# Kernel tuning notes

Measured on AMD Instinct MI355X. Metric: run time of the kernel, lower is better.

The kernel has to match this reference:

```python
import jax, jax.numpy as jnp
import numpy as np

B = 65536
PEP, TCR, D, FF = 384, 480, 128, 512
H1, H2, OUT = 128, 64, 1
EPS = 1e-5


def _ln(x, g, b):
    mu = jnp.mean(x, axis=-1, keepdims=True)
    var = jnp.mean((x - mu) ** 2, axis=-1, keepdims=True)
    return (x - mu) * jax.lax.rsqrt(var + EPS) * g + b


def _bn(x, g, b):
    # training-mode BatchNorm1d: batch-wide stats, biased variance
    mu = jnp.mean(x, axis=0, keepdims=True)
    var = jnp.mean((x - mu) ** 2, axis=0, keepdims=True)
    return (x - mu) * jax.lax.rsqrt(var + EPS) * g + b


def setup_inputs() -> dict:
    key = jax.random.key(0)
    ks = iter(jax.random.split(key, 40))

    def w(shape, fan):
        s = float(np.sqrt(6.0 / fan))
        return jax.random.uniform(next(ks), shape, jnp.float32, -s, s)

    inp = {
        "x": jax.random.normal(next(ks), (B, PEP + TCR), jnp.float32),
        "w_pep": w((D, PEP), PEP + D), "b_pep": jnp.zeros(D),
        "w_tcr": w((D, TCR), TCR + D), "b_tcr": jnp.zeros(D),
        "wv_p2t": w((D, D), 2 * D), "bv_p2t": jnp.zeros(D),
        "wo_p2t": w((D, D), 2 * D), "bo_p2t": jnp.zeros(D),
        "wv_t2p": w((D, D), 2 * D), "bv_t2p": jnp.zeros(D),
        "wo_t2p": w((D, D), 2 * D), "bo_t2p": jnp.zeros(D),
        "ln_g1p": jnp.ones(D), "ln_b1p": jnp.zeros(D),
        "ln_g2p": jnp.ones(D), "ln_b2p": jnp.zeros(D),
        "ln_g1t": jnp.ones(D), "ln_b1t": jnp.zeros(D),
        "ln_g2t": jnp.ones(D), "ln_b2t": jnp.zeros(D),
        "ffn_w1p": w((FF, D), D + FF), "ffn_b1p": jnp.zeros(FF),
        "ffn_w2p": w((D, FF), D + FF), "ffn_b2p": jnp.zeros(D),
        "ffn_w1t": w((FF, D), D + FF), "ffn_b1t": jnp.zeros(FF),
        "ffn_w2t": w((D, FF), D + FF), "ffn_b2t": jnp.zeros(D),
        "w_h1": w((H1, 2 * D), 2 * D + H1), "b_h1": jnp.zeros(H1),
        "bn1_g": jnp.ones(H1), "bn1_b": jnp.zeros(H1),
        "w_h2": w((H2, H1), H1 + H2), "b_h2": jnp.zeros(H2),
        "bn2_g": jnp.ones(H2), "bn2_b": jnp.zeros(H2),
        "w_out": w((OUT, H2), H2 + OUT), "b_out": jnp.zeros(OUT),
    }
    return inp


def reference(x, w_pep, b_pep, w_tcr, b_tcr,
              wv_p2t, bv_p2t, wo_p2t, bo_p2t,
              wv_t2p, bv_t2p, wo_t2p, bo_t2p,
              ln_g1p, ln_b1p, ln_g2p, ln_b2p,
              ln_g1t, ln_b1t, ln_g2t, ln_b2t,
              ffn_w1p, ffn_b1p, ffn_w2p, ffn_b2p,
              ffn_w1t, ffn_b1t, ffn_w2t, ffn_b2t,
              w_h1, b_h1, bn1_g, bn1_b,
              w_h2, b_h2, bn2_g, bn2_b,
              w_out, b_out):
    pep = x[:, :PEP] @ w_pep.T + b_pep   # (B, 128)
    tcr = x[:, PEP:] @ w_tcr.T + b_tcr   # (B, 128)

    # MHA with seq_len=1: softmax over single key == 1 exactly,
    # so attention output = out_proj(v_proj(key/value input)).
    pa = (tcr @ wv_p2t.T + bv_p2t) @ wo_p2t.T + bo_p2t
    pa = _ln(pep + pa, ln_g1p, ln_b1p)
    h = jax.nn.gelu(pa @ ffn_w1p.T + ffn_b1p, approximate=False)
    pa = _ln(pa + h @ ffn_w2p.T + ffn_b2p, ln_g2p, ln_b2p)

    ta = (pep @ wv_t2p.T + bv_t2p) @ wo_t2p.T + bo_t2p
    ta = _ln(tcr + ta, ln_g1t, ln_b1t)
    h = jax.nn.gelu(ta @ ffn_w1t.T + ffn_b1t, approximate=False)
    ta = _ln(ta + h @ ffn_w2t.T + ffn_b2t, ln_g2t, ln_b2t)

    combined = jnp.concatenate([pa, ta], axis=1)  # (B, 256)
    h1 = jax.nn.gelu(_bn(combined @ w_h1.T + b_h1, bn1_g, bn1_b), approximate=False)
    h2 = jax.nn.gelu(_bn(h1 @ w_h2.T + b_h2, bn2_g, bn2_b), approximate=False)
    return h2 @ w_out.T + b_out  # (B, 1)
```

## Files before the change

kernel.cpp:

```cpp
#include <hip/hip_runtime.h>
#include <hip/hip_bf16.h>
#include <math.h>


typedef __attribute__((ext_vector_type(8))) __bf16 bf16x8;
typedef __attribute__((ext_vector_type(8))) short s16x8;
typedef __attribute__((ext_vector_type(4))) float f32x4;

union S8U { s16x8 s; bf16x8 b; };

__device__ __forceinline__ short f2b(float f) {
  union { float f; unsigned u; } v; v.f = f;
  unsigned r = v.u + 0x7fffu + ((v.u >> 16) & 1u);
  return (short)(r >> 16);
}
__device__ __forceinline__ float b2f(short s) {
  union { unsigned u; float f; } v; v.u = ((unsigned)(unsigned short)s) << 16;
  return v.f;
}
__device__ __forceinline__ float gelu_f(float x) {
  return 0.5f * x * (1.0f + erff(x * 0.7071067811865475f));
}

template<int NTS>
__device__ __forceinline__ void mfma_step(const short* __restrict__ Abuf, int lda, int kkA,
                                          const short* __restrict__ W, int ldw, int kw,
                                          int colbase, int l16, int q,
                                          f32x4 (&acc)[4][NTS]) {
  S8U a[4];
#pragma unroll
  for (int mt = 0; mt < 4; ++mt)
    a[mt].s = *(const s16x8*)(Abuf + (16 * mt + l16) * lda + kkA + 8 * q);
#pragma unroll
  for (int nt = 0; nt < NTS; ++nt) {
    S8U b;
    b.s = *(const s16x8*)(W + (size_t)(colbase + 16 * nt + l16) * ldw + kw + 8 * q);
#pragma unroll
    for (int mt = 0; mt < 4; ++mt)
      acc[mt][nt] = __builtin_amdgcn_mfma_f32_16x16x32_bf16(a[mt].b, b.b, acc[mt][nt], 0, 0, 0);
  }
}

template<int NTS>
__device__ __forceinline__ void zero_acc(f32x4 (&acc)[4][NTS]) {
  f32x4 z = {0.f, 0.f, 0.f, 0.f};
#pragma unroll
  for (int mt = 0; mt < 4; ++mt)
#pragma unroll
    for (int nt = 0; nt < NTS; ++nt) acc[mt][nt] = z;
}

__device__ __forceinline__ void epi_bias_store(f32x4 (&acc)[4][2], const float* __restrict__ bias,
                                               short* dst, int w, int l16, int q, bool do_gelu) {
#pragma unroll
  for (int nt = 0; nt < 2; ++nt) {
    int col = 32 * w + 16 * nt + l16;
    float bb = bias[col];
#pragma unroll
    for (int mt = 0; mt < 4; ++mt)
#pragma unroll
      for (int r = 0; r < 4; ++r) {
        int row = 16 * mt + 4 * q + r;
        float v = acc[mt][nt][r] + bb;
        if (do_gelu) v = gelu_f(v);
        dst[row * 136 + col] = f2b(v);
      }
  }
}

__device__ __forceinline__ void epi_res_ln(f32x4 (&acc)[4][2], const float* __restrict__ bias,
                                           const short* resbuf,
                                           const float* __restrict__ g, const float* __restrict__ bta,
                                           short* dst, float (*lnp)[4][2], float (*murs)[2],
                                           int w, int l16, int q, int tid) {
#pragma unroll
  for (int nt = 0; nt < 2; ++nt) {
    int col = 32 * w + 16 * nt + l16;
    float bb = bias[col];
#pragma unroll
    for (int mt = 0; mt < 4; ++mt)
#pragma unroll
      for (int r = 0; r < 4; ++r) {
        int row = 16 * mt + 4 * q + r;
        acc[mt][nt][r] += bb + b2f(resbuf[row * 136 + col]);
      }
  }
#pragma unroll
  for (int mt = 0; mt < 4; ++mt) {
#pragma unroll
    for (int r = 0; r < 4; ++r) {
      float v0 = acc[mt][0][r], v1 = acc[mt][1][r];
      float s = v0 + v1;
      float sq = v0 * v0 + v1 * v1;
#pragma unroll
      for (int off = 1; off < 16; off <<= 1) {
        s += __shfl_xor(s, off);
        sq += __shfl_xor(sq, off);
      }
      if (l16 == 0) {
        int row = 16 * mt + 4 * q + r;
        lnp[row][w][0] = s;
        lnp[row][w][1] = sq;
      }
    }
  }
  __syncthreads();
  if (tid < 64) {
    float s = lnp[tid][0][0] + lnp[tid][1][0] + lnp[tid][2][0] + lnp[tid][3][0];
    float sq = lnp[tid][0][1] + lnp[tid][1][1] + lnp[tid][2][1] + lnp[tid][3][1];
    float mu = s * (1.0f / 128.0f);
    float var = sq * (1.0f / 128.0f) - mu * mu;
    murs[tid][0] = mu;
    murs[tid][1] = rsqrtf(var + 1e-5f);
  }
  __syncthreads();
#pragma unroll
  for (int nt = 0; nt < 2; ++nt) {
    int col = 32 * w + 16 * nt + l16;
    float gg = g[col], b2 = bta[col];
#pragma unroll
    for (int mt = 0; mt < 4; ++mt)
#pragma unroll
      for (int r = 0; r < 4; ++r) {
        int row = 16 * mt + 4 * q + r;
        float v = (acc[mt][nt][r] - murs[row][0]) * murs[row][1] * gg + b2;
        dst[row * 136 + col] = f2b(v);
      }
  }
}

__device__ __forceinline__ void ffn_block(const short* __restrict__ w1, const short* __restrict__ w2,
                                          const float* __restrict__ b1, const float* __restrict__ b2,
                                          const float* __restrict__ g, const float* __restrict__ bta,
                                          short* act, short* H,
                                          float (*lnp)[4][2], float (*murs)[2],
                                          int w, int l16, int q, int tid) {
  f32x4 acc2[4][2];
  zero_acc(acc2);
  for (int c = 0; c < 4; ++c) {
    f32x4 acch[4][2];
    zero_acc(acch);
#pragma unroll
    for (int kk = 0; kk < 4; ++kk)
      mfma_step<2>(act, 136, 32 * kk, w1, 128, 32 * kk, c * 128 + 32 * w, l16, q, acch);
#pragma unroll
    for (int nt = 0; nt < 2; ++nt) {
      int lcol = 32 * w + 16 * nt + l16;
      float bb = b1[c * 128 + lcol];
#pragma unroll
      for (int mt = 0; mt < 4; ++mt)
#pragma unroll
        for (int r = 0; r < 4; ++r)
          H[(16 * mt + 4 * q + r) * 136 + lcol] = f2b(gelu_f(acch[mt][nt][r] + bb));
    }
    __syncthreads();
#pragma unroll
    for (int kk = 0; kk < 4; ++kk)
      mfma_step<2>(H, 136, 32 * kk, w2, 512, c * 128 + 32 * kk, 32 * w, l16, q, acc2);
    __syncthreads();
  }
  epi_res_ln(acc2, b2, act, g, bta, act, lnp, murs, w, l16, q, tid);
}

struct K1Args {
  const float* x;
  const short *wpep, *wtcr, *wvp, *wop, *wvt, *wot, *w1p, *w2p, *w1t, *w2t, *wh1;
  const float *bpep, *btcr, *bvp, *bop, *bvt, *bot;
  const float *g1p, *e1p, *g2p, *e2p, *g1t, *e1t, *g2t, *e2t;
  const float *b1p, *b2p, *b1t, *b2t, *bh1;
  float *sum1, *sq1;
  short* h1;
};

__global__ __launch_bounds__(256, 2) void k1_main(K1Args A) {
  __shared__ __align__(16) short smem[4 * 64 * 136 + 2 * 64 * 40];
  short* U = smem;
  short* V = U + 64 * 136;
  short* T = V + 64 * 136;
  short* H = T + 64 * 136;
  short* S = H + 64 * 136;
  float (*lnp)[4][2] = (float (*)[4][2])(void*)S;
  float (*murs)[2] = (float (*)[2])(void*)(S + 1024);

  const int tid = threadIdx.x;
  const int w = tid >> 6;
  const int lane = tid & 63;
  const int l16 = lane & 15;
  const int q = lane >> 4;
  const size_t row0 = (size_t)blockIdx.x * 64;

  auto stage = [&](int kbase, short* Sb) {
    int r = tid >> 2, c8 = (tid & 3) * 8;
    const float* p = A.x + (row0 + r) * 864 + kbase + c8;
    float4 f0 = *(const float4*)p;
    float4 f1 = *(const float4*)(p + 4);
    s16x8 o;
    o[0] = f2b(f0.x); o[1] = f2b(f0.y); o[2] = f2b(f0.z); o[3] = f2b(f0.w);
    o[4] = f2b(f1.x); o[5] = f2b(f1.y); o[6] = f2b(f1.z); o[7] = f2b(f1.w);
    *(s16x8*)(Sb + r * 40 + c8) = o;
  };

  f32x4 acc[4][2];

  zero_acc(acc);
  for (int t = 0; t < 12; ++t) {
    stage(32 * t, S + (t & 1) * (64 * 40));
    __syncthreads();
    mfma_step<2>(S + (t & 1) * (64 * 40), 40, 0, A.wpep, 384, 32 * t, 32 * w, l16, q, acc);
  }
  epi_bias_store(acc, A.bpep, U, w, l16, q, false);

  zero_acc(acc);
  for (int t = 0; t < 15; ++t) {
    stage(384 + 32 * t, S + (t & 1) * (64 * 40));
    __syncthreads();
    mfma_step<2>(S + (t & 1) * (64 * 40), 40, 0, A.wtcr, 480, 32 * t, 32 * w, l16, q, acc);
  }
  epi_bias_store(acc, A.btcr, V, w, l16, q, false);
  __syncthreads();

  zero_acc(acc);
#pragma unroll
  for (int kk = 0; kk < 4; ++kk)
    mfma_step<2>(V, 136, 32 * kk, A.wvp, 128, 32 * kk, 32 * w, l16, q, acc);
  epi_bias_store(acc, A.bvp, T, w, l16, q, false);

  zero_acc(acc);
#pragma unroll
  for (int kk = 0; kk < 4; ++kk)
    mfma_step<2>(U, 136, 32 * kk, A.wvt, 128, 32 * kk, 32 * w, l16, q, acc);
  epi_bias_store(acc, A.bvt, H, w, l16, q, false);
  __syncthreads();

  zero_acc(acc);
#pragma unroll
  for (int kk = 0; kk < 4; ++kk)
    mfma_step<2>(T, 136, 32 * kk, A.wop, 128, 32 * kk, 32 * w, l16, q, acc);
  epi_res_ln(acc, A.bop, U, A.g1p, A.e1p, U, lnp, murs, w, l16, q, tid);

  zero_acc(acc);
#pragma unroll
  for (int kk = 0; kk < 4; ++kk)
    mfma_step<2>(H, 136, 32 * kk, A.wot, 128, 32 * kk, 32 * w, l16, q, acc);
  epi_res_ln(acc, A.bot, V, A.g1t, A.e1t, V, lnp, murs, w, l16, q, tid);

  ffn_block(A.w1p, A.w2p, A.b1p, A.b2p, A.g2p, A.e2p, U, H, lnp, murs, w, l16, q, tid);
  ffn_block(A.w1t, A.w2t, A.b1t, A.b2t, A.g2t, A.e2t, V, H, lnp, murs, w, l16, q, tid);
  __syncthreads();

  zero_acc(acc);
#pragma unroll
  for (int s = 0; s < 8; ++s)
    mfma_step<2>((s < 4) ? U : V, 136, 32 * (s & 3), A.wh1, 256, 32 * s, 32 * w, l16, q, acc);
#pragma unroll
  for (int nt = 0; nt < 2; ++nt) {
    int col = 32 * w + 16 * nt + l16;
    float bb = A.bh1[col];
    float s = 0.f, sq = 0.f;
#pragma unroll
    for (int mt = 0; mt < 4; ++mt)
#pragma unroll
      for (int r = 0; r < 4; ++r) {
        float v = acc[mt][nt][r] + bb;
        s += v; sq += v * v;
        A.h1[(row0 + 16 * mt + 4 * q + r) * 128 + col] = f2b(v);
      }
    s += __shfl_xor(s, 16); sq += __shfl_xor(sq, 16);
    s += __shfl_xor(s, 32); sq += __shfl_xor(sq, 32);
    if (q == 0) {
      atomicAdd(&A.sum1[col], s);
      atomicAdd(&A.sq1[col], sq);
    }
  }
}

struct K2Args {
  const short* h1;
  const short* wh2;
  const float *bh2, *bn1g, *bn1b;
  const float *sum1, *sq1;
  float *sum2, *sq2;
  short* h2;
};

__global__ __launch_bounds__(256) void k2_main(K2Args A) {
  __shared__ __align__(16) short S2[64 * 136];
  __shared__ float s1[128], t1[128];
  const int tid = threadIdx.x;
  const int w = tid >> 6, lane = tid & 63, l16 = lane & 15, q = lane >> 4;
  const size_t row0 = (size_t)blockIdx.x * 64;

  if (tid < 128) {
    float su = A.sum1[tid], sq = A.sq1[tid];
    float mu = su * (1.0f / 65536.0f);
    float var = sq * (1.0f / 65536.0f) - mu * mu;
    float sc = A.bn1g[tid] * rsqrtf(var + 1e-5f);
    s1[tid] = sc;
    t1[tid] = A.bn1b[tid] - mu * sc;
  }
  __syncthreads();
  {
    int r = tid >> 2;
#pragma unroll
    for (int j = 0; j < 4; ++j) {
      int c = (tid & 3) * 32 + j * 8;
      s16x8 hv = *(const s16x8*)(A.h1 + (row0 + r) * 128 + c);
      s16x8 o;
#pragma unroll
      for (int i = 0; i < 8; ++i) {
        float f = b2f(hv[i]);
        f = gelu_f(f * s1[c + i] + t1[c + i]);
        o[i] = f2b(f);
      }
      *(s16x8*)(S2 + r * 136 + c) = o;
    }
  }
  __syncthreads();
  f32x4 acc[4][1];
  zero_acc(acc);
#pragma unroll
  for (int kk = 0; kk < 4; ++kk)
    mfma_step<1>(S2, 136, 32 * kk, A.wh2, 128, 32 * kk, 16 * w, l16, q, acc);
  int col = 16 * w + l16;
  float bb = A.bh2[col];
  float s = 0.f, sq = 0.f;
#pragma unroll
  for (int mt = 0; mt < 4; ++mt)
#pragma unroll
    for (int r = 0; r < 4; ++r) {
      float v = acc[mt][0][r] + bb;
      s += v; sq += v * v;
      A.h2[(row0 + 16 * mt + 4 * q + r) * 64 + col] = f2b(v);
    }
  s += __shfl_xor(s, 16); sq += __shfl_xor(sq, 16);
  s += __shfl_xor(s, 32); sq += __shfl_xor(sq, 32);
  if (q == 0) {
    atomicAdd(&A.sum2[col], s);
    atomicAdd(&A.sq2[col], sq);
  }
}

struct K3Args {
  const short* h2;
  const float *bn2g, *bn2b;
  const float *sum2, *sq2;
  const float *wout, *bout;
  float* out;
};

__global__ __launch_bounds__(256) void k3_main(K3Args A) {
  __shared__ float s2[64], t2[64], wo[64];
  const int tid = threadIdx.x;
  if (tid < 64) {
    float su = A.sum2[tid], sq = A.sq2[tid];
    float mu = su * (1.0f / 65536.0f);
    float var = sq * (1.0f / 65536.0f) - mu * mu;
    float sc = A.bn2g[tid] * rsqrtf(var + 1e-5f);
    s2[tid] = sc;
    t2[tid] = A.bn2b[tid] - mu * sc;
    wo[tid] = A.wout[tid];
  }
  __syncthreads();
  size_t row = (size_t)blockIdx.x * 32 + (tid >> 3);
  int c0 = (tid & 7) * 8;
  s16x8 hv = *(const s16x8*)(A.h2 + row * 64 + c0);
  float s = 0.f;
#pragma unroll
  for (int i = 0; i < 8; ++i) {
    float f = b2f(hv[i]);
    f = gelu_f(f * s2[c0 + i] + t2[c0 + i]);
    s += f * wo[c0 + i];
  }
  s += __shfl_xor(s, 1); s += __shfl_xor(s, 2); s += __shfl_xor(s, 4);
  if ((tid & 7) == 0) A.out[row] = s + A.bout[0];
}

struct CvtArgs {
  const float* src[12];
  short* dst;
  float* stats;
};

__global__ __launch_bounds__(256) void k0_setup(CvtArgs A) {
  const int cum[13] = {0, 49152, 110592, 126976, 143360, 159744, 176128,
                       241664, 307200, 372736, 438272, 471040, 479232};
  int b = blockIdx.x;
  if (b == 0) {
    A.stats[threadIdx.x] = 0.0f;
    if (threadIdx.x < 128) A.stats[256 + threadIdx.x] = 0.0f;
  }
  int base = b * 1024;
  int seg = 0;
#pragma unroll
  for (int t = 1; t < 12; ++t) seg += (base >= cum[t]) ? 1 : 0;
  const float* s = A.src[seg];
  int loc = base - cum[seg] + threadIdx.x * 4;
  float4 f = *(const float4*)(s + loc);
  int di = base + threadIdx.x * 4;
  A.dst[di + 0] = f2b(f.x);
  A.dst[di + 1] = f2b(f.y);
  A.dst[di + 2] = f2b(f.z);
  A.dst[di + 3] = f2b(f.w);
}

extern "C" void kernel_launch(void* const* d_in, const int* in_sizes, int n_in,
                              void* d_out, int out_size, void* d_ws, size_t ws_size,
                              hipStream_t stream) {
  (void)in_sizes; (void)n_in; (void)out_size; (void)ws_size;
  const float* x = (const float*)d_in[0];
  char* ws = (char*)d_ws;
  short* wb = (short*)ws;
  enum { O_PEP = 0, O_TCR = 49152, O_VP2T = 110592, O_OP2T = 126976,
         O_VT2P = 143360, O_OT2P = 159744, O_W1P = 176128, O_W2P = 241664,
         O_W1T = 307200, O_W2T = 372736, O_H1 = 438272, O_H2 = 471040 };
  float* stats = (float*)(ws + 958464);
  short* h1_pre = (short*)(ws + 960000);
  short* h2_pre = (short*)(ws + 17737216);

  CvtArgs ca;
  ca.src[0]  = (const float*)d_in[1];
  ca.src[1]  = (const float*)d_in[3];
  ca.src[2]  = (const float*)d_in[5];
  ca.src[3]  = (const float*)d_in[7];
  ca.src[4]  = (const float*)d_in[9];
  ca.src[5]  = (const float*)d_in[11];
  ca.src[6]  = (const float*)d_in[21];
  ca.src[7]  = (const float*)d_in[23];
  ca.src[8]  = (const float*)d_in[25];
  ca.src[9]  = (const float*)d_in[27];
  ca.src[10] = (const float*)d_in[29];
  ca.src[11] = (const float*)d_in[33];
  ca.dst = wb;
  ca.stats = stats;
  k0_setup<<<468, 256, 0, stream>>>(ca);

  K1Args a1;
  a1.x = x;
  a1.wpep = wb + O_PEP;  a1.wtcr = wb + O_TCR;
  a1.wvp = wb + O_VP2T;  a1.wop = wb + O_OP2T;
  a1.wvt = wb + O_VT2P;  a1.wot = wb + O_OT2P;
  a1.w1p = wb + O_W1P;   a1.w2p = wb + O_W2P;
  a1.w1t = wb + O_W1T;   a1.w2t = wb + O_W2T;
  a1.wh1 = wb + O_H1;
  a1.bpep = (const float*)d_in[2];
  a1.btcr = (const float*)d_in[4];
  a1.bvp = (const float*)d_in[6];
  a1.bop = (const float*)d_in[8];
  a1.bvt = (const float*)d_in[10];
  a1.bot = (const float*)d_in[12];
  a1.g1p = (const float*)d_in[13];  a1.e1p = (const float*)d_in[14];
  a1.g2p = (const float*)d_in[15];  a1.e2p = (const float*)d_in[16];
  a1.g1t = (const float*)d_in[17];  a1.e1t = (const float*)d_in[18];
  a1.g2t = (const float*)d_in[19];  a1.e2t = (const float*)d_in[20];
  a1.b1p = (const float*)d_in[22];
  a1.b2p = (const float*)d_in[24];
  a1.b1t = (const float*)d_in[26];
  a1.b2t = (const float*)d_in[28];
  a1.bh1 = (const float*)d_in[30];
  a1.sum1 = stats;
  a1.sq1 = stats + 128;
  a1.h1 = h1_pre;
  k1_main<<<1024, 256, 0, stream>>>(a1);

  K2Args a2;
  a2.h1 = h1_pre;
  a2.wh2 = wb + O_H2;
  a2.bh2 = (const float*)d_in[34];
  a2.bn1g = (const float*)d_in[31];
  a2.bn1b = (const float*)d_in[32];
  a2.sum1 = stats;
  a2.sq1 = stats + 128;
  a2.sum2 = stats + 256;
  a2.sq2 = stats + 320;
  a2.h2 = h2_pre;
  k2_main<<<1024, 256, 0, stream>>>(a2);

  K3Args a3;
  a3.h2 = h2_pre;
  a3.bn2g = (const float*)d_in[35];
  a3.bn2b = (const float*)d_in[36];
  a3.sum2 = stats + 256;
  a3.sq2 = stats + 320;
  a3.wout = (const float*)d_in[37];
  a3.bout = (const float*)d_in[38];
  a3.out = (float*)d_out;
  k3_main<<<2048, 256, 0, stream>>>(a3);
}
```

Before: 594.0 us.

## Restructure pipeline into single-wave 16-row kernels with tanh GELU and sliced stats

Replaces the 256-thread, 64-row main kernel with a separate input-projection kernel and a one-wavefront-per-16-rows body kernel. Each wave computes all 128 output columns, so the block-wide syncthreads and LDS LayerNorm reduction are no longer needed. Erf GELU becomes a tanh/exp approximation, and conversions use packed bf16 instructions. BatchNorm statistics are spread over 16 atomic slices to reduce contention. The trade-offs are an extra intermediate buffer written to and read from global memory and the small numerical error of the approximate GELU.

New measurement: 867.5 us. 1.46x slower.

```diff
diff --git a/kernel.cpp b/kernel.cpp
--- a/kernel.cpp
+++ b/kernel.cpp
@@ -4,10 +4,17 @@
 
 
 typedef __attribute__((ext_vector_type(8))) __bf16 bf16x8;
+typedef __attribute__((ext_vector_type(2))) __bf16 bf16x2;
 typedef __attribute__((ext_vector_type(8))) short s16x8;
 typedef __attribute__((ext_vector_type(4))) float f32x4;
 
-union S8U { s16x8 s; bf16x8 b; };
+union S8U { s16x8 s; bf16x8 b; int i[4]; };
+
+#if defined(__has_builtin)
+#if __has_builtin(__builtin_amdgcn_cvt_pk_bf16_f32)
+#define HAVE_PK_BF16 1
+#endif
+#endif
 
 __device__ __forceinline__ short f2b(float f) {
   union { float f; unsigned u; } v; v.f = f;
@@ -18,343 +25,341 @@
   union { unsigned u; float f; } v; v.u = ((unsigned)(unsigned short)s) << 16;
   return v.f;
 }
+__device__ __forceinline__ int cvt2(float lo, float hi) {
+#ifdef HAVE_PK_BF16
+  union { bf16x2 v; int i; } u;
+  u.v = __builtin_amdgcn_cvt_pk_bf16_f32(lo, hi);
+  return u.i;
+#else
+  return ((int)(unsigned short)f2b(lo)) | (((int)(unsigned short)f2b(hi)) << 16);
+#endif
+}
+__device__ __forceinline__ s16x8 pack8(const float* a) {
+  union { s16x8 s; int i[4]; } u;
+  u.i[0] = cvt2(a[0], a[1]); u.i[1] = cvt2(a[2], a[3]);
+  u.i[2] = cvt2(a[4], a[5]); u.i[3] = cvt2(a[6], a[7]);
+  return u.s;
+}
 __device__ __forceinline__ float gelu_f(float x) {
-  return 0.5f * x * (1.0f + erff(x * 0.7071067811865475f));
-}
-
-template<int NTS>
-__device__ __forceinline__ void mfma_step(const short* __restrict__ Abuf, int lda, int kkA,
-                                          const short* __restrict__ W, int ldw, int kw,
-                                          int colbase, int l16, int q,
-                                          f32x4 (&acc)[4][NTS]) {
-  S8U a[4];
-#pragma unroll
-  for (int mt = 0; mt < 4; ++mt)
-    a[mt].s = *(const s16x8*)(Abuf + (16 * mt + l16) * lda + kkA + 8 * q);
-#pragma unroll
-  for (int nt = 0; nt < NTS; ++nt) {
-    S8U b;
-    b.s = *(const s16x8*)(W + (size_t)(colbase + 16 * nt + l16) * ldw + kw + 8 * q);
-#pragma unroll
-    for (int mt = 0; mt < 4; ++mt)
-      acc[mt][nt] = __builtin_amdgcn_mfma_f32_16x16x32_bf16(a[mt].b, b.b, acc[mt][nt], 0, 0, 0);
-  }
-}
-
-template<int NTS>
-__device__ __forceinline__ void zero_acc(f32x4 (&acc)[4][NTS]) {
+  float u = x * (0.7978845608028654f + 0.035677408136300125f * x * x);
+  float e = __expf(2.0f * u);
+  float t = 1.0f - 2.0f / (e + 1.0f);
+  return 0.5f * x * (1.0f + t);
+}
+
+__device__ __forceinline__ f32x4 mfma_bf16(const S8U& a, const S8U& b, f32x4 c) {
+  return __builtin_amdgcn_mfma_f32_16x16x32_bf16(a.b, b.b, c, 0, 0, 0);
+}
+
+template<int NKT, int NC>
+__device__ __forceinline__ void gemm_w(const short* __restrict__ buf,
+                                       const short* __restrict__ W, int ldw,
+                                       int wc0, int kw0, int l16, int q,
+                                       f32x4 (&acc)[NC]) {
+#pragma unroll
+  for (int kt = 0; kt < NKT; ++kt) {
+    S8U a; a.s = *(const s16x8*)(buf + l16 * 136 + 32 * kt + 8 * q);
+#pragma unroll
+    for (int n = 0; n < NC; ++n) {
+      S8U b;
+      b.s = *(const s16x8*)(W + (size_t)(wc0 + 16 * n + l16) * ldw + kw0 + 32 * kt + 8 * q);
+      acc[n] = mfma_bf16(a, b, acc[n]);
+    }
+  }
+}
+
+template<int NC>
+__device__ __forceinline__ void zero_acc(f32x4 (&acc)[NC]) {
   f32x4 z = {0.f, 0.f, 0.f, 0.f};
 #pragma unroll
-  for (int mt = 0; mt < 4; ++mt)
-#pragma unroll
-    for (int nt = 0; nt < NTS; ++nt) acc[mt][nt] = z;
-}
-
-__device__ __forceinline__ void epi_bias_store(f32x4 (&acc)[4][2], const float* __restrict__ bias,
-                                               short* dst, int w, int l16, int q, bool do_gelu) {
-#pragma unroll
-  for (int nt = 0; nt < 2; ++nt) {
-    int col = 32 * w + 16 * nt + l16;
+  for (int n = 0; n < NC; ++n) acc[n] = z;
+}
+
+__device__ __forceinline__ void store_c(const f32x4 (&acc)[8], const float* __restrict__ bias,
+                                        short* dst, int l16, int q, bool do_gelu) {
+#pragma unroll
+  for (int n = 0; n < 8; ++n) {
+    int col = 16 * n + l16;
     float bb = bias[col];
 #pragma unroll
-    for (int mt = 0; mt < 4; ++mt)
-#pragma unroll
-      for (int r = 0; r < 4; ++r) {
-        int row = 16 * mt + 4 * q + r;
-        float v = acc[mt][nt][r] + bb;
-        if (do_gelu) v = gelu_f(v);
-        dst[row * 136 + col] = f2b(v);
-      }
-  }
-}
-
-__device__ __forceinline__ void epi_res_ln(f32x4 (&acc)[4][2], const float* __restrict__ bias,
-                                           const short* resbuf,
-                                           const float* __restrict__ g, const float* __restrict__ bta,
-                                           short* dst, float (*lnp)[4][2], float (*murs)[2],
-                                           int w, int l16, int q, int tid) {
-#pragma unroll
-  for (int nt = 0; nt < 2; ++nt) {
-    int col = 32 * w + 16 * nt + l16;
-    float bb = bias[col];
-#pragma unroll
-    for (int mt = 0; mt < 4; ++mt)
-#pragma unroll
-      for (int r = 0; r < 4; ++r) {
-        int row = 16 * mt + 4 * q + r;
-        acc[mt][nt][r] += bb + b2f(resbuf[row * 136 + col]);
-      }
-  }
-#pragma unroll
-  for (int mt = 0; mt < 4; ++mt) {
-#pragma unroll
     for (int r = 0; r < 4; ++r) {
-      float v0 = acc[mt][0][r], v1 = acc[mt][1][r];
-      float s = v0 + v1;
-      float sq = v0 * v0 + v1 * v1;
-#pragma unroll
-      for (int off = 1; off < 16; off <<= 1) {
-        s += __shfl_xor(s, off);
-        sq += __shfl_xor(sq, off);
-      }
-      if (l16 == 0) {
-        int row = 16 * mt + 4 * q + r;
-        lnp[row][w][0] = s;
-        lnp[row][w][1] = sq;
-      }
-    }
-  }
-  __syncthreads();
-  if (tid < 64) {
-    float s = lnp[tid][0][0] + lnp[tid][1][0] + lnp[tid][2][0] + lnp[tid][3][0];
-    float sq = lnp[tid][0][1] + lnp[tid][1][1] + lnp[tid][2][1] + lnp[tid][3][1];
+      float v = acc[n][r] + bb;
+      if (do_gelu) v = gelu_f(v);
+      dst[(4 * q + r) * 136 + col] = f2b(v);
+    }
+  }
+}
+
+__device__ __forceinline__ void res_ln(f32x4 (&acc)[8], const float* __restrict__ bias,
+                                       short* buf, const float* __restrict__ g,
+                                       const float* __restrict__ bt, int l16, int q) {
+  float gg[8], bb[8];
+#pragma unroll
+  for (int n = 0; n < 8; ++n) {
+    int col = 16 * n + l16;
+    float bv = bias[col];
+    gg[n] = g[col]; bb[n] = bt[col];
+#pragma unroll
+    for (int r = 0; r < 4; ++r)
+      acc[n][r] += bv + b2f(buf[(4 * q + r) * 136 + col]);
+  }
+#pragma unroll
+  for (int r = 0; r < 4; ++r) {
+    float s = 0.f, sq = 0.f;
+#pragma unroll
+    for (int n = 0; n < 8; ++n) { float v = acc[n][r]; s += v; sq += v * v; }
+#pragma unroll
+    for (int m = 1; m < 16; m <<= 1) { s += __shfl_xor(s, m); sq += __shfl_xor(sq, m); }
     float mu = s * (1.0f / 128.0f);
     float var = sq * (1.0f / 128.0f) - mu * mu;
-    murs[tid][0] = mu;
-    murs[tid][1] = rsqrtf(var + 1e-5f);
-  }
-  __syncthreads();
-#pragma unroll
-  for (int nt = 0; nt < 2; ++nt) {
-    int col = 32 * w + 16 * nt + l16;
-    float gg = g[col], b2 = bta[col];
-#pragma unroll
-    for (int mt = 0; mt < 4; ++mt)
-#pragma unroll
-      for (int r = 0; r < 4; ++r) {
-        int row = 16 * mt + 4 * q + r;
-        float v = (acc[mt][nt][r] - murs[row][0]) * murs[row][1] * gg + b2;
-        dst[row * 136 + col] = f2b(v);
+    float rs = rsqrtf(var + 1e-5f);
+#pragma unroll
+    for (int n = 0; n < 8; ++n)
+      buf[(4 * q + r) * 136 + 16 * n + l16] = f2b((acc[n][r] - mu) * rs * gg[n] + bb[n]);
+  }
+}
+
+__device__ __forceinline__ void ffn(short* act, short* S1,
+                                    const short* __restrict__ w1, const float* __restrict__ b1,
+                                    const short* __restrict__ w2, const float* __restrict__ b2,
+                                    const float* __restrict__ g, const float* __restrict__ bt,
+                                    int l16, int q) {
+  f32x4 acc2[8];
+  zero_acc(acc2);
+#pragma unroll 1
+  for (int c = 0; c < 4; ++c) {
+    f32x4 h[8];
+    zero_acc(h);
+    gemm_w<4, 8>(act, w1, 128, 128 * c, 0, l16, q, h);
+    store_c(h, b1 + 128 * c, S1, l16, q, true);
+    gemm_w<4, 8>(S1, w2, 512, 0, 128 * c, l16, q, acc2);
+  }
+  res_ln(acc2, b2, act, g, bt, l16, q);
+}
+
+struct KaArgs {
+  const float* x;
+  const short *wpep, *wtcr;
+  const float *bpep, *btcr;
+  short* pt;
+};
+
+__global__ __launch_bounds__(64, 3) void ka_proj(KaArgs A) {
+  const int lane = threadIdx.x;
+  const int l16 = lane & 15, q = lane >> 4;
+  const size_t R0 = (size_t)blockIdx.x * 16;
+  const float* xp = A.x + (R0 + l16) * 864 + 8 * q;
+
+  f32x4 acc[16];
+  zero_acc(acc);
+
+  float4 c0 = *(const float4*)(xp);
+  float4 c1 = *(const float4*)(xp + 4);
+#pragma unroll 1
+  for (int t = 0; t < 27; ++t) {
+    float4 n0 = c0, n1 = c1;
+    if (t < 26) {
+      n0 = *(const float4*)(xp + 32 * (t + 1));
+      n1 = *(const float4*)(xp + 32 * (t + 1) + 4);
+    }
+    float av[8] = {c0.x, c0.y, c0.z, c0.w, c1.x, c1.y, c1.z, c1.w};
+    S8U af; af.s = pack8(av);
+    if (t < 12) {
+      const short* W = A.wpep + l16 * 384 + 32 * t + 8 * q;
+#pragma unroll
+      for (int n = 0; n < 8; ++n) {
+        S8U b; b.s = *(const s16x8*)(W + (size_t)n * 16 * 384);
+        acc[n] = mfma_bf16(af, b, acc[n]);
       }
-  }
-}
-
-__device__ __forceinline__ void ffn_block(const short* __restrict__ w1, const short* __restrict__ w2,
-                                          const float* __restrict__ b1, const float* __restrict__ b2,
-                                          const float* __restrict__ g, const float* __restrict__ bta,
-                                          short* act, short* H,
-                                          float (*lnp)[4][2], float (*murs)[2],
-                                          int w, int l16, int q, int tid) {
-  f32x4 acc2[4][2];
-  zero_acc(acc2);
-  for (int c = 0; c < 4; ++c) {
-    f32x4 acch[4][2];
-    zero_acc(acch);
-#pragma unroll
-    for (int kk = 0; kk < 4; ++kk)
-      mfma_step<2>(act, 136, 32 * kk, w1, 128, 32 * kk, c * 128 + 32 * w, l16, q, acch);
-#pragma unroll
-    for (int nt = 0; nt < 2; ++nt) {
-      int lcol = 32 * w + 16 * nt + l16;
-      float bb = b1[c * 128 + lcol];
-#pragma unroll
-      for (int mt = 0; mt < 4; ++mt)
-#pragma unroll
-        for (int r = 0; r < 4; ++r)
-          H[(16 * mt + 4 * q + r) * 136 + lcol] = f2b(gelu_f(acch[mt][nt][r] + bb));
-    }
-    __syncthreads();
-#pragma unroll
-    for (int kk = 0; kk < 4; ++kk)
-      mfma_step<2>(H, 136, 32 * kk, w2, 512, c * 128 + 32 * kk, 32 * w, l16, q, acc2);
-    __syncthreads();
-  }
-  epi_res_ln(acc2, b2, act, g, bta, act, lnp, murs, w, l16, q, tid);
-}
-
-struct K1Args {
-  const float* x;
-  const short *wpep, *wtcr, *wvp, *wop, *wvt, *wot, *w1p, *w2p, *w1t, *w2t, *wh1;
-  const float *bpep, *btcr, *bvp, *bop, *bvt, *bot;
+    } else {
+      const short* W = A.wtcr + l16 * 480 + 32 * (t - 12) + 8 * q;
+#pragma unroll
+      for (int n = 0; n < 8; ++n) {
+        S8U b; b.s = *(const s16x8*)(W + (size_t)n * 16 * 480);
+        acc[8 + n] = mfma_bf16(af, b, acc[8 + n]);
+      }
+    }
+    c0 = n0; c1 = n1;
+  }
+  short* ptp = A.pt + (R0 + 4 * q) * 256;
+#pragma unroll
+  for (int n = 0; n < 16; ++n) {
+    int col = 16 * n + l16;
+    float bb = (n < 8) ? A.bpep[col] : A.btcr[col - 128];
+#pragma unroll
+    for (int r = 0; r < 4; ++r)
+      ptp[(size_t)r * 256 + col] = f2b(acc[n][r] + bb);
+  }
+}
+
+struct KbArgs {
+  const short* pt;
+  const short *wvp, *wop, *wvt, *wot, *w1p, *w2p, *w1t, *w2t, *wh1;
+  const float *bvp, *bop, *bvt, *bot;
   const float *g1p, *e1p, *g2p, *e2p, *g1t, *e1t, *g2t, *e2t;
   const float *b1p, *b2p, *b1t, *b2t, *bh1;
-  float *sum1, *sq1;
+  float* stats;
   short* h1;
 };
 
-__global__ __launch_bounds__(256, 2) void k1_main(K1Args A) {
-  __shared__ __align__(16) short smem[4 * 64 * 136 + 2 * 64 * 40];
-  short* U = smem;
-  short* V = U + 64 * 136;
-  short* T = V + 64 * 136;
-  short* H = T + 64 * 136;
-  short* S = H + 64 * 136;
-  float (*lnp)[4][2] = (float (*)[4][2])(void*)S;
-  float (*murs)[2] = (float (*)[2])(void*)(S + 1024);
-
-  const int tid = threadIdx.x;
-  const int w = tid >> 6;
-  const int lane = tid & 63;
-  const int l16 = lane & 15;
-  const int q = lane >> 4;
-  const size_t row0 = (size_t)blockIdx.x * 64;
-
-  auto stage = [&](int kbase, short* Sb) {
-    int r = tid >> 2, c8 = (tid & 3) * 8;
-    const float* p = A.x + (row0 + r) * 864 + kbase + c8;
-    float4 f0 = *(const float4*)p;
-    float4 f1 = *(const float4*)(p + 4);
-    s16x8 o;
-    o[0] = f2b(f0.x); o[1] = f2b(f0.y); o[2] = f2b(f0.z); o[3] = f2b(f0.w);
-    o[4] = f2b(f1.x); o[5] = f2b(f1.y); o[6] = f2b(f1.z); o[7] = f2b(f1.w);
-    *(s16x8*)(Sb + r * 40 + c8) = o;
-  };
-
-  f32x4 acc[4][2];
-
+__global__ __launch_bounds__(64, 3) void kb_body(KbArgs A) {
+  __shared__ __align__(16) short L[3 * 16 * 136];
+  short* U = L;
+  short* V = L + 16 * 136;
+  short* S1 = L + 2 * 16 * 136;
+  const int lane = threadIdx.x;
+  const int l16 = lane & 15, q = lane >> 4;
+  const size_t R0 = (size_t)blockIdx.x * 16;
+
+  {
+    const short* p = A.pt + (R0 + l16) * 256 + 64 * q;
+#pragma unroll
+    for (int jj = 0; jj < 8; ++jj) {
+      s16x8 vv = *(const s16x8*)(p + 8 * jj);
+      int c = 64 * q + 8 * jj;
+      if (q < 2) *(s16x8*)(U + l16 * 136 + c) = vv;
+      else       *(s16x8*)(V + l16 * 136 + c - 128) = vv;
+    }
+  }
+
+  f32x4 accT[8], accH[8];
+  zero_acc(accT); zero_acc(accH);
+  gemm_w<4, 8>(V, A.wvp, 128, 0, 0, l16, q, accT);
+  gemm_w<4, 8>(U, A.wvt, 128, 0, 0, l16, q, accH);
+
+  f32x4 acc[8];
+  store_c(accT, A.bvp, S1, l16, q, false);
   zero_acc(acc);
-  for (int t = 0; t < 12; ++t) {
-    stage(32 * t, S + (t & 1) * (64 * 40));
-    __syncthreads();
-    mfma_step<2>(S + (t & 1) * (64 * 40), 40, 0, A.wpep, 384, 32 * t, 32 * w, l16, q, acc);
-  }
-  epi_bias_store(acc, A.bpep, U, w, l16, q, false);
-
+  gemm_w<4, 8>(S1, A.wop, 128, 0, 0, l16, q, acc);
+  res_ln(acc, A.bop, U, A.g1p, A.e1p, l16, q);
+  store_c(accH, A.bvt, S1, l16, q, false);
   zero_acc(acc);
-  for (int t = 0; t < 15; ++t) {
-    stage(384 + 32 * t, S + (t & 1) * (64 * 40));
-    __syncthreads();
-    mfma_step<2>(S + (t & 1) * (64 * 40), 40, 0, A.wtcr, 480, 32 * t, 32 * w, l16, q, acc);
-  }
-  epi_bias_store(acc, A.btcr, V, w, l16, q, false);
-  __syncthreads();
+  gemm_w<4, 8>(S1, A.wot, 128, 0, 0, l16, q, acc);
+  res_ln(acc, A.bot, V, A.g1t, A.e1t, l16, q);
+
+  ffn(U, S1, A.w1p, A.b1p, A.w2p, A.b2p, A.g2p, A.e2p, l16, q);
+  ffn(V, S1, A.w1t, A.b1t, A.w2t, A.b2t, A.g2t, A.e2t, l16, q);
 
   zero_acc(acc);
-#pragma unroll
-  for (int kk = 0; kk < 4; ++kk)
-    mfma_step<2>(V, 136, 32 * kk, A.wvp, 128, 32 * kk, 32 * w, l16, q, acc);
-  epi_bias_store(acc, A.bvp, T, w, l16, q, false);
-
-  zero_acc(acc);
-#pragma unroll
-  for (int kk = 0; kk < 4; ++kk)
-    mfma_step<2>(U, 136, 32 * kk, A.wvt, 128, 32 * kk, 32 * w, l16, q, acc);
-  epi_bias_store(acc, A.bvt, H, w, l16, q, false);
-  __syncthreads();
-
-  zero_acc(acc);
-#pragma unroll
-  for (int kk = 0; kk < 4; ++kk)
-    mfma_step<2>(T, 136, 32 * kk, A.wop, 128, 32 * kk, 32 * w, l16, q, acc);
-  epi_res_ln(acc, A.bop, U, A.g1p, A.e1p, U, lnp, murs, w, l16, q, tid);
-
-  zero_acc(acc);
-#pragma unroll
-  for (int kk = 0; kk < 4; ++kk)
-    mfma_step<2>(H, 136, 32 * kk, A.wot, 128, 32 * kk, 32 * w, l16, q, acc);
-  epi_res_ln(acc, A.bot, V, A.g1t, A.e1t, V, lnp, murs, w, l16, q, tid);
-
-  ffn_block(A.w1p, A.w2p, A.b1p, A.b2p, A.g2p, A.e2p, U, H, lnp, murs, w, l16, q, tid);
-  ffn_block(A.w1t, A.w2t, A.b1t, A.b2t, A.g2t, A.e2t, V, H, lnp, murs, w, l16, q, tid);
-  __syncthreads();
-
-  zero_acc(acc);
-#pragma unroll
-  for (int s = 0; s < 8; ++s)
-    mfma_step<2>((s < 4) ? U : V, 136, 32 * (s & 3), A.wh1, 256, 32 * s, 32 * w, l16, q, acc);
-#pragma unroll
-  for (int nt = 0; nt < 2; ++nt) {
-    int col = 32 * w + 16 * nt + l16;
+  gemm_w<4, 8>(U, A.wh1, 256, 0, 0, l16, q, acc);
+  gemm_w<4, 8>(V, A.wh1, 256, 0, 128, l16, q, acc);
+  const int slice = blockIdx.x & 15;
+  short* hp = A.h1 + (R0 + 4 * q) * 128;
+#pragma unroll
+  for (int n = 0; n < 8; ++n) {
+    int col = 16 * n + l16;
     float bb = A.bh1[col];
     float s = 0.f, sq = 0.f;
 #pragma unroll
-    for (int mt = 0; mt < 4; ++mt)
-#pragma unroll
-      for (int r = 0; r < 4; ++r) {
-        float v = acc[mt][nt][r] + bb;
-        s += v; sq += v * v;
-        A.h1[(row0 + 16 * mt + 4 * q + r) * 128 + col] = f2b(v);
-      }
+    for (int r = 0; r < 4; ++r) {
+      float v = acc[n][r] + bb;
+      s += v; sq += v * v;
+      hp[(size_t)r * 128 + col] = f2b(v);
+    }
     s += __shfl_xor(s, 16); sq += __shfl_xor(sq, 16);
     s += __shfl_xor(s, 32); sq += __shfl_xor(sq, 32);
     if (q == 0) {
-      atomicAdd(&A.sum1[col], s);
-      atomicAdd(&A.sq1[col], sq);
-    }
-  }
-}
-
-struct K2Args {
+      atomicAdd(&A.stats[slice * 128 + col], s);
+      atomicAdd(&A.stats[2048 + slice * 128 + col], sq);
+    }
+  }
+}
+
+struct KcArgs {
   const short* h1;
   const short* wh2;
   const float *bh2, *bn1g, *bn1b;
-  const float *sum1, *sq1;
-  float *sum2, *sq2;
+  float* stats;
   short* h2;
 };
 
-__global__ __launch_bounds__(256) void k2_main(K2Args A) {
-  __shared__ __align__(16) short S2[64 * 136];
+__global__ __launch_bounds__(64, 4) void kc_bn1(KcArgs A) {
   __shared__ float s1[128], t1[128];
-  const int tid = threadIdx.x;
-  const int w = tid >> 6, lane = tid & 63, l16 = lane & 15, q = lane >> 4;
-  const size_t row0 = (size_t)blockIdx.x * 64;
-
-  if (tid < 128) {
-    float su = A.sum1[tid], sq = A.sq1[tid];
-    float mu = su * (1.0f / 65536.0f);
-    float var = sq * (1.0f / 65536.0f) - mu * mu;
-    float sc = A.bn1g[tid] * rsqrtf(var + 1e-5f);
-    s1[tid] = sc;
-    t1[tid] = A.bn1b[tid] - mu * sc;
-  }
-  __syncthreads();
-  {
-    int r = tid >> 2;
-#pragma unroll
-    for (int j = 0; j < 4; ++j) {
-      int c = (tid & 3) * 32 + j * 8;
-      s16x8 hv = *(const s16x8*)(A.h1 + (row0 + r) * 128 + c);
-      s16x8 o;
-#pragma unroll
-      for (int i = 0; i < 8; ++i) {
-        float f = b2f(hv[i]);
-        f = gelu_f(f * s1[c + i] + t1[c + i]);
-        o[i] = f2b(f);
-      }
-      *(s16x8*)(S2 + r * 136 + c) = o;
-    }
-  }
-  __syncthreads();
-  f32x4 acc[4][1];
+  const int lane = threadIdx.x;
+  const int l16 = lane & 15, q = lane >> 4;
+  const size_t R0 = (size_t)blockIdx.x * 16;
+
+#pragma unroll
+  for (int j = 0; j < 2; ++j) {
+    int c = 2 * lane + j;
+    float S = 0.f, Q = 0.f;
+#pragma unroll
+    for (int s = 0; s < 16; ++s) {
+      S += A.stats[s * 128 + c];
+      Q += A.stats[2048 + s * 128 + c];
+    }
+    float mu = S * (1.0f / 65536.0f);
+    float var = Q * (1.0f / 65536.0f) - mu * mu;
+    float sc = A.bn1g[c] * rsqrtf(var + 1e-5f);
+    s1[c] = sc;
+    t1[c] = A.bn1b[c] - mu * sc;
+  }
+
+  f32x4 acc[4];
   zero_acc(acc);
-#pragma unroll
-  for (int kk = 0; kk < 4; ++kk)
-    mfma_step<1>(S2, 136, 32 * kk, A.wh2, 128, 32 * kk, 16 * w, l16, q, acc);
-  int col = 16 * w + l16;
-  float bb = A.bh2[col];
-  float s = 0.f, sq = 0.f;
-#pragma unroll
-  for (int mt = 0; mt < 4; ++mt)
+  const short* hp = A.h1 + (R0 + l16) * 128 + 8 * q;
+#pragma unroll
+  for (int kt = 0; kt < 4; ++kt) {
+    S8U gv; gv.s = *(const s16x8*)(hp + 32 * kt);
+    f32x4 sA = *(const f32x4*)(s1 + 32 * kt + 8 * q);
+    f32x4 sB = *(const f32x4*)(s1 + 32 * kt + 8 * q + 4);
+    f32x4 tA = *(const f32x4*)(t1 + 32 * kt + 8 * q);
+    f32x4 tB = *(const f32x4*)(t1 + 32 * kt + 8 * q + 4);
+    float av[8];
+#pragma unroll
+    for (int i = 0; i < 4; ++i) av[i] = gelu_f(b2f(gv.s[i]) * sA[i] + tA[i]);
+#pragma unroll
+    for (int i = 0; i < 4; ++i) av[4 + i] = gelu_f(b2f(gv.s[4 + i]) * sB[i] + tB[i]);
+    S8U f; f.s = pack8(av);
+    const short* W = A.wh2 + l16 * 128 + 32 * kt + 8 * q;
+#pragma unroll
+    for (int n = 0; n < 4; ++n) {
+      S8U b; b.s = *(const s16x8*)(W + (size_t)n * 16 * 128);
+      acc[n] = mfma_bf16(f, b, acc[n]);
+    }
+  }
+  const int slice = blockIdx.x & 15;
+  short* op = A.h2 + (R0 + 4 * q) * 64;
+#pragma unroll
+  for (int n = 0; n < 4; ++n) {
+    int col = 16 * n + l16;
+    float bb = A.bh2[col];
+    float s = 0.f, sq = 0.f;
 #pragma unroll
     for (int r = 0; r < 4; ++r) {
-      float v = acc[mt][0][r] + bb;
+      float v = acc[n][r] + bb;
       s += v; sq += v * v;
-      A.h2[(row0 + 16 * mt + 4 * q + r) * 64 + col] = f2b(v);
-    }
-  s += __shfl_xor(s, 16); sq += __shfl_xor(sq, 16);
-  s += __shfl_xor(s, 32); sq += __shfl_xor(sq, 32);
-  if (q == 0) {
-    atomicAdd(&A.sum2[col], s);
-    atomicAdd(&A.sq2[col], sq);
-  }
-}
-
-struct K3Args {
+      op[(size_t)r * 64 + col] = f2b(v);
+    }
+    s += __shfl_xor(s, 16); sq += __shfl_xor(sq, 16);
+    s += __shfl_xor(s, 32); sq += __shfl_xor(sq, 32);
+    if (q == 0) {
+      atomicAdd(&A.stats[4096 + slice * 64 + col], s);
+      atomicAdd(&A.stats[5120 + slice * 64 + col], sq);
+    }
+  }
+}
+
+struct KdArgs {
   const short* h2;
   const float *bn2g, *bn2b;
-  const float *sum2, *sq2;
+  const float* stats;
   const float *wout, *bout;
   float* out;
 };
 
-__global__ __launch_bounds__(256) void k3_main(K3Args A) {
+__global__ __launch_bounds__(256) void kd_out(KdArgs A) {
   __shared__ float s2[64], t2[64], wo[64];
   const int tid = threadIdx.x;
   if (tid < 64) {
-    float su = A.sum2[tid], sq = A.sq2[tid];
-    float mu = su * (1.0f / 65536.0f);
-    float var = sq * (1.0f / 65536.0f) - mu * mu;
+    float S = 0.f, Q = 0.f;
+#pragma unroll
+    for (int s = 0; s < 16; ++s) {
+      S += A.stats[4096 + s * 64 + tid];
+      Q += A.stats[5120 + s * 64 + tid];
+    }
+    float mu = S * (1.0f / 65536.0f);
+    float var = Q * (1.0f / 65536.0f) - mu * mu;
     float sc = A.bn2g[tid] * rsqrtf(var + 1e-5f);
     s2[tid] = sc;
     t2[tid] = A.bn2b[tid] - mu * sc;
@@ -367,8 +372,7 @@
   float s = 0.f;
 #pragma unroll
   for (int i = 0; i < 8; ++i) {
-    float f = b2f(hv[i]);
-    f = gelu_f(f * s2[c0 + i] + t2[c0 + i]);
+    float f = gelu_f(b2f(hv[i]) * s2[c0 + i] + t2[c0 + i]);
     s += f * wo[c0 + i];
   }
   s += __shfl_xor(s, 1); s += __shfl_xor(s, 2); s += __shfl_xor(s, 4);
@@ -385,10 +389,7 @@
   const int cum[13] = {0, 49152, 110592, 126976, 143360, 159744, 176128,
                        241664, 307200, 372736, 438272, 471040, 479232};
   int b = blockIdx.x;
-  if (b == 0) {
-    A.stats[threadIdx.x] = 0.0f;
-    if (threadIdx.x < 128) A.stats[256 + threadIdx.x] = 0.0f;
-  }
+  if (b < 24) A.stats[b * 256 + threadIdx.x] = 0.0f;
   int base = b * 1024;
   int seg = 0;
 #pragma unroll
@@ -397,25 +398,25 @@
   int loc = base - cum[seg] + threadIdx.x * 4;
   float4 f = *(const float4*)(s + loc);
   int di = base + threadIdx.x * 4;
-  A.dst[di + 0] = f2b(f.x);
-  A.dst[di + 1] = f2b(f.y);
-  A.dst[di + 2] = f2b(f.z);
-  A.dst[di + 3] = f2b(f.w);
+  int2 p;
+  p.x = cvt2(f.x, f.y);
+  p.y = cvt2(f.z, f.w);
+  *(int2*)(A.dst + di) = p;
 }
 
 extern "C" void kernel_launch(void* const* d_in, const int* in_sizes, int n_in,
                               void* d_out, int out_size, void* d_ws, size_t ws_size,
                               hipStream_t stream) {
   (void)in_sizes; (void)n_in; (void)out_size; (void)ws_size;
-  const float* x = (const float*)d_in[0];
   char* ws = (char*)d_ws;
   short* wb = (short*)ws;
   enum { O_PEP = 0, O_TCR = 49152, O_VP2T = 110592, O_OP2T = 126976,
          O_VT2P = 143360, O_OT2P = 159744, O_W1P = 176128, O_W2P = 241664,
          O_W1T = 307200, O_W2T = 372736, O_H1 = 438272, O_H2 = 471040 };
-  float* stats = (float*)(ws + 958464);
-  short* h1_pre = (short*)(ws + 960000);
-  short* h2_pre = (short*)(ws + 17737216);
+  float* stats  = (float*)(ws + 958464);
+  short* pt     = (short*)(ws + 983040);
+  short* h1_pre = (short*)(ws + 34537472);
+  short* h2_pre = (short*)(ws + 983040);
 
   CvtArgs ca;
   ca.src[0]  = (const float*)d_in[1];
@@ -434,55 +435,55 @@
   ca.stats = stats;
   k0_setup<<<468, 256, 0, stream>>>(ca);
 
-  K1Args a1;
-  a1.x = x;
-  a1.wpep = wb + O_PEP;  a1.wtcr = wb + O_TCR;
-  a1.wvp = wb + O_VP2T;  a1.wop = wb + O_OP2T;
-  a1.wvt = wb + O_VT2P;  a1.wot = wb + O_OT2P;
-  a1.w1p = wb + O_W1P;   a1.w2p = wb + O_W2P;
-  a1.w1t = wb + O_W1T;   a1.w2t = wb + O_W2T;
-  a1.wh1 = wb + O_H1;
-  a1.bpep = (const float*)d_in[2];
-  a1.btcr = (const float*)d_in[4];
-  a1.bvp = (const float*)d_in[6];
-  a1.bop = (const float*)d_in[8];
-  a1.bvt = (const float*)d_in[10];
-  a1.bot = (const float*)d_in[12];
-  a1.g1p = (const float*)d_in[13];  a1.e1p = (const float*)d_in[14];
-  a1.g2p = (const float*)d_in[15];  a1.e2p = (const float*)d_in[16];
-  a1.g1t = (const float*)d_in[17];  a1.e1t = (const float*)d_in[18];
-  a1.g2t = (const float*)d_in[19];  a1.e2t = (const float*)d_in[20];
-  a1.b1p = (const float*)d_in[22];
-  a1.b2p = (const float*)d_in[24];
-  a1.b1t = (const float*)d_in[26];
-  a1.b2t = (const float*)d_in[28];
-  a1.bh1 = (const float*)d_in[30];
-  a1.sum1 = stats;
-  a1.sq1 = stats + 128;
-  a1.h1 = h1_pre;
-  k1_main<<<1024, 256, 0, stream>>>(a1);
-
-  K2Args a2;
-  a2.h1 = h1_pre;
-  a2.wh2 = wb + O_H2;
-  a2.bh2 = (const float*)d_in[34];
-  a2.bn1g = (const float*)d_in[31];
-  a2.bn1b = (const float*)d_in[32];
-  a2.sum1 = stats;
-  a2.sq1 = stats + 128;
-  a2.sum2 = stats + 256;
-  a2.sq2 = stats + 320;
-  a2.h2 = h2_pre;
-  k2_main<<<1024, 256, 0, stream>>>(a2);
-
-  K3Args a3;
-  a3.h2 = h2_pre;
-  a3.bn2g = (const float*)d_in[35];
-  a3.bn2b = (const float*)d_in[36];
-  a3.sum2 = stats + 256;
-  a3.sq2 = stats + 320;
-  a3.wout = (const float*)d_in[37];
-  a3.bout = (const float*)d_in[38];
-  a3.out = (float*)d_out;
-  k3_main<<<2048, 256, 0, stream>>>(a3);
-}
+  KaArgs a;
+  a.x = (const float*)d_in[0];
+  a.wpep = wb + O_PEP; a.wtcr = wb + O_TCR;
+  a.bpep = (const float*)d_in[2];
+  a.btcr = (const float*)d_in[4];
+  a.pt = pt;
+  ka_proj<<<4096, 64, 0, stream>>>(a);
+
+  KbArgs b;
+  b.pt = pt;
+  b.wvp = wb + O_VP2T; b.wop = wb + O_OP2T;
+  b.wvt = wb + O_VT2P; b.wot = wb + O_OT2P;
+  b.w1p = wb + O_W1P;  b.w2p = wb + O_W2P;
+  b.w1t = wb + O_W1T;  b.w2t = wb + O_W2T;
+  b.wh1 = wb + O_H1;
+  b.bvp = (const float*)d_in[6];
+  b.bop = (const float*)d_in[8];
+  b.bvt = (const float*)d_in[10];
+  b.bot = (const float*)d_in[12];
+  b.g1p = (const float*)d_in[13]; b.e1p = (const float*)d_in[14];
+  b.g2p = (const float*)d_in[15]; b.e2p = (const float*)d_in[16];
+  b.g1t = (const float*)d_in[17]; b.e1t = (const float*)d_in[18];
+  b.g2t = (const float*)d_in[19]; b.e2t = (const float*)d_in[20];
+  b.b1p = (const float*)d_in[22];
+  b.b2p = (const float*)d_in[24];
+  b.b1t = (const float*)d_in[26];
+  b.b2t = (const float*)d_in[28];
+  b.bh1 = (const float*)d_in[30];
+  b.stats = stats;
+  b.h1 = h1_pre;
+  kb_body<<<4096, 64, 0, stream>>>(b);
+
+  KcArgs c;
+  c.h1 = h1_pre;
+  c.wh2 = wb + O_H2;
+  c.bh2 = (const float*)d_in[34];
+  c.bn1g = (const float*)d_in[31];
+  c.bn1b = (const float*)d_in[32];
+  c.stats = stats;
+  c.h2 = h2_pre;
+  kc_bn1<<<4096, 64, 0, stream>>>(c);
+
+  KdArgs d;
+  d.h2 = h2_pre;
+  d.bn2g = (const float*)d_in[35];
+  d.bn2b = (const float*)d_in[36];
+  d.stats = stats;
+  d.wout = (const float*)d_in[37];
+  d.bout = (const float*)d_in[38];
+  d.out = (float*)d_out;
+  kd_out<<<2048, 256, 0, stream>>>(d);
+}
```
